# Kernel optimization log

Measured on AMD Instinct MI355X. Metric: run time of the kernel, lower is better.

Reference implementation:

```python
import jax, jax.numpy as jnp
import numpy as np

B, T, N, F_IN = 4, 8, 2048, 16
HID, HEADS, OUT_CH, OUT_FEAT = 128, 4, 64, 14
E = 32768


def _ln(x, g, b, eps=1e-5):
    mu = x.mean(-1, keepdims=True)
    var = ((x - mu) ** 2).mean(-1, keepdims=True)
    return (x - mu) / jnp.sqrt(var + eps) * g + b


def _attn_steps(x, wq, bq, wk, bk, wv, bv, wo, bo):
    # x: [B, S, M, F]; single-head causal attention over axis 1 (the 'steps' axis)
    q = x @ wq + bq
    k = x @ wk + bk
    v = x @ wv + bv
    scale = 1.0 / np.sqrt(q.shape[-1]).astype(np.float32)
    scores = jnp.einsum('bsmh,btmh->bmst', q, k) * scale  # [B,M,S,S]
    S = scores.shape[-1]
    scores = jnp.where(jnp.tril(jnp.ones((S, S), bool)), scores, -jnp.inf)
    a = jax.nn.softmax(scores, axis=-1)
    ctx = jnp.einsum('bmst,btmh->bsmh', a, v)
    return ctx @ wo + bo


def _attn_nodes(x, wq, bq, wk, bk, wv, bv, wo, bo):
    # single-head attention over axis 2 (the 'nodes' axis)
    q = x @ wq + bq
    k = x @ wk + bk
    v = x @ wv + bv
    scale = 1.0 / np.sqrt(q.shape[-1]).astype(np.float32)
    scores = jnp.einsum('bsnh,bsmh->bsnm', q, k) * scale
    a = jax.nn.softmax(scores, axis=-1)
    ctx = jnp.einsum('bsnm,bsmh->bsnh', a, v)
    return ctx @ wo + bo


def _gat(h, src, dst, n, W, a_src, a_dst, bias, heads, out_ch, concat):
    # PyG GATConv: gather src/dst features per edge, segment softmax over
    # incoming edges of each target node, weighted scatter-aggregate.
    hw = (h @ W).reshape(n, heads, out_ch)
    al_s = (hw * a_src).sum(-1)  # [n, heads]
    al_d = (hw * a_dst).sum(-1)
    loop = jnp.arange(n, dtype=src.dtype)
    src_f = jnp.concatenate([src, loop])
    dst_f = jnp.concatenate([dst, loop])
    alpha = jax.nn.leaky_relu(al_s[src_f] + al_d[dst_f], 0.2)
    # PyG removes pre-existing self-loops then adds canonical ones: mask them out.
    drop = jnp.concatenate([src == dst, jnp.zeros((n,), bool)])[:, None]
    amax = jax.lax.stop_gradient(
        jax.ops.segment_max(jnp.where(drop, -jnp.inf, alpha), dst_f, num_segments=n))
    ex = jnp.where(drop, 0.0, jnp.exp(alpha - amax[dst_f]))
    denom = jax.ops.segment_sum(ex, dst_f, num_segments=n)
    w = ex / denom[dst_f]  # [E_total, heads]
    out = jax.ops.segment_sum(hw[src_f] * w[:, :, None], dst_f, num_segments=n)
    if concat:
        return out.reshape(n, heads * out_ch) + bias
    return out.mean(1) + bias


def _forward(x, edge_index, ln1_g, ln1_b, t_wq, t_bq, t_wk, t_bk, t_wv, t_bv, t_wo, t_bo,
             skip_w, skip_b, ln2_g, ln2_b, s_wq, s_bq, s_wk, s_bk, s_wv, s_bv, s_wo, s_bo,
             ln3_g, ln3_b, mlp_w1, mlp_b1, mlp_w2, mlp_b2,
             gat1_w, gat1_asrc, gat1_adst, gat1_b, gat2_w, gat2_asrc, gat2_adst, gat2_b,
             ffn_w, ffn_b):
    Bx, Tx, Nx, _ = x.shape
    h = jnp.transpose(x, (0, 2, 1, 3))  # [B, N(steps), T(nodes), F]
    h = (h @ skip_w + skip_b) + _attn_steps(_ln(h, ln1_g, ln1_b),
                                            t_wq, t_bq, t_wk, t_bk, t_wv, t_bv, t_wo, t_bo)
    h = h + _attn_nodes(_ln(h, ln2_g, ln2_b), s_wq, s_bq, s_wk, s_bk, s_wv, s_bv, s_wo, s_bo)
    z = _ln(h, ln3_g, ln3_b)
    h = h + (jax.nn.relu(z @ mlp_w1 + mlp_b1) @ mlp_w2 + mlp_b2)
    h = h[:, :, -1, :].reshape(Bx * Nx, HID)  # last 'nodes'(=T) slot, flatten graphs
    src, dst = edge_index[0], edge_index[1]
    off = jnp.repeat(jnp.arange(Bx, dtype=src.dtype) * Nx, src.shape[0])
    src_b = jnp.tile(src, Bx) + off
    dst_b = jnp.tile(dst, Bx) + off
    nt = Bx * Nx
    g1 = jax.nn.elu(_gat(h, src_b, dst_b, nt, gat1_w, gat1_asrc, gat1_adst, gat1_b,
                         HEADS, HID // HEADS, True))
    g2 = _gat(g1, src_b, dst_b, nt, gat2_w, gat2_asrc, gat2_adst, gat2_b, 1, OUT_CH, False)
    out = g2.reshape(Bx, Nx, OUT_CH) @ ffn_w + ffn_b
    return jnp.transpose(out, (0, 2, 1))  # [B, output_features, N]


def setup_inputs():
    key = jax.random.key(0)
    ki = iter(list(jax.random.split(key, 40)))
    def rn(shape, s=0.05):
        return jax.random.normal(next(ki), shape, jnp.float32) * s
    d = {}
    d['x'] = jax.random.normal(next(ki), (B, T, N, F_IN), jnp.float32)
    d['edge_index'] = jax.random.randint(next(ki), (2, E), 0, N, jnp.int32)
    d['ln1_g'] = jnp.ones((F_IN,), jnp.float32); d['ln1_b'] = jnp.zeros((F_IN,), jnp.float32)
    d['t_wq'] = rn((F_IN, HID)); d['t_bq'] = jnp.zeros((HID,), jnp.float32)
    d['t_wk'] = rn((F_IN, HID)); d['t_bk'] = jnp.zeros((HID,), jnp.float32)
    d['t_wv'] = rn((F_IN, HID)); d['t_bv'] = jnp.zeros((HID,), jnp.float32)
    d['t_wo'] = rn((HID, HID)); d['t_bo'] = jnp.zeros((HID,), jnp.float32)
    d['skip_w'] = rn((F_IN, HID)); d['skip_b'] = jnp.zeros((HID,), jnp.float32)
    d['ln2_g'] = jnp.ones((HID,), jnp.float32); d['ln2_b'] = jnp.zeros((HID,), jnp.float32)
    d['s_wq'] = rn((HID, HID)); d['s_bq'] = jnp.zeros((HID,), jnp.float32)
    d['s_wk'] = rn((HID, HID)); d['s_bk'] = jnp.zeros((HID,), jnp.float32)
    d['s_wv'] = rn((HID, HID)); d['s_bv'] = jnp.zeros((HID,), jnp.float32)
    d['s_wo'] = rn((HID, HID)); d['s_bo'] = jnp.zeros((HID,), jnp.float32)
    d['ln3_g'] = jnp.ones((HID,), jnp.float32); d['ln3_b'] = jnp.zeros((HID,), jnp.float32)
    d['mlp_w1'] = rn((HID, 2 * HID)); d['mlp_b1'] = jnp.zeros((2 * HID,), jnp.float32)
    d['mlp_w2'] = rn((2 * HID, HID)); d['mlp_b2'] = jnp.zeros((HID,), jnp.float32)
    d['gat1_w'] = rn((HID, HID))
    d['gat1_asrc'] = rn((HEADS, HID // HEADS)); d['gat1_adst'] = rn((HEADS, HID // HEADS))
    d['gat1_b'] = jnp.zeros((HID,), jnp.float32)
    d['gat2_w'] = rn((HID, OUT_CH))
    d['gat2_asrc'] = rn((1, OUT_CH)); d['gat2_adst'] = rn((1, OUT_CH))
    d['gat2_b'] = jnp.zeros((OUT_CH,), jnp.float32)
    d['ffn_w'] = rn((OUT_CH, OUT_FEAT)); d['ffn_b'] = jnp.zeros((OUT_FEAT,), jnp.float32)
    return d


def reference(x, edge_index, ln1_g, ln1_b, t_wq, t_bq, t_wk, t_bk, t_wv, t_bv, t_wo, t_bo,
              skip_w, skip_b, ln2_g, ln2_b, s_wq, s_bq, s_wk, s_bk, s_wv, s_bv, s_wo, s_bo,
              ln3_g, ln3_b, mlp_w1, mlp_b1, mlp_w2, mlp_b2,
              gat1_w, gat1_asrc, gat1_adst, gat1_b, gat2_w, gat2_asrc, gat2_adst, gat2_b,
              ffn_w, ffn_b):
    return _forward(x, edge_index, ln1_g, ln1_b, t_wq, t_bq, t_wk, t_bk, t_wv, t_bv, t_wo, t_bo,
                    skip_w, skip_b, ln2_g, ln2_b, s_wq, s_bq, s_wk, s_bk, s_wv, s_bv, s_wo, s_bo,
                    ln3_g, ln3_b, mlp_w1, mlp_b1, mlp_w2, mlp_b2,
                    gat1_w, gat1_asrc, gat1_adst, gat1_b, gat2_w, gat2_asrc, gat2_adst, gat2_b,
                    ffn_w, ffn_b)
```

## Files before the change

### kernel.cpp

```cpp
#include <hip/hip_runtime.h>
#include <hip/hip_bf16.h>
#include <stdint.h>


#define BB     4
#define TT     8
#define NN     2048
#define FIN    16
#define HID    128
#define BM     (BB*TT)
#define PROWS  (BM*NN)
#define NHEADS 4
#define OUTCH  64
#define OUTF   14
#define NEDGE  32768
#define NEDGEB (NEDGE*BB)
#define NNODE  (BB*NN)
#define NETOT  (NEDGEB + NNODE)

#define TQ     64
#define NTILE  (NN/TQ)

typedef __hip_bfloat16 bf16;
typedef __attribute__((ext_vector_type(8))) short bf16x8;
typedef __attribute__((ext_vector_type(4))) float f32x4;

__device__ __forceinline__ float b2f(bf16 v){ return __bfloat162float(v); }
__device__ __forceinline__ bf16  f2b(float f){ return __float2bfloat16(f); }
__device__ __forceinline__ unsigned short bfbits(float f){
    union { bf16 h; unsigned short u; } cv; cv.h = f2b(f); return cv.u;
}

__global__ __launch_bounds__(256)
void k_kv(const float* __restrict__ x,
          const float* __restrict__ g1, const float* __restrict__ bb1,
          const float* __restrict__ wk, const float* __restrict__ bk,
          const float* __restrict__ wv, const float* __restrict__ bv,
          int in_off, bf16* __restrict__ K, bf16* __restrict__ Vt)
{
    const int r0 = blockIdx.x * 32;
    const int t  = threadIdx.x;

    __shared__ float wk_s[FIN][HID];
    __shared__ float wv_s[FIN][HID];
    __shared__ float xr_s[32][FIN+1];
    __shared__ float ln_s[32][FIN+1];

    #pragma unroll
    for (int it = 0; it < 2; ++it){
        const int u = t + it*256;
        ((float4*)wk_s)[u] = ((const float4*)wk)[u];
        ((float4*)wv_s)[u] = ((const float4*)wv)[u];
    }
    #pragma unroll
    for (int it = 0; it < 2; ++it){
        const int u = t + it*256;
        xr_s[u >> 4][u & 15] = x[(size_t)(r0 + in_off)*FIN + u];
    }
    __syncthreads();

    if (t < 32){
        float mu = 0.f;
        #pragma unroll
        for (int f = 0; f < FIN; ++f) mu += xr_s[t][f];
        mu *= (1.f/FIN);
        float var = 0.f;
        #pragma unroll
        for (int f = 0; f < FIN; ++f){ float d = xr_s[t][f]-mu; var += d*d; }
        var *= (1.f/FIN);
        const float inv = rsqrtf(var + 1e-5f);
        #pragma unroll
        for (int f = 0; f < FIN; ++f)
            ln_s[t][f] = (xr_s[t][f]-mu)*inv*g1[f] + bb1[f];
    }
    __syncthreads();

    {
        const int hk = (t & 63)*2;
        const float2 bkv = *(const float2*)&bk[hk];
        #pragma unroll
        for (int pass = 0; pass < 8; ++pass){
            const int key = pass*4 + (t >> 6);
            float a0 = bkv.x, a1 = bkv.y;
            #pragma unroll
            for (int f = 0; f < FIN; ++f){
                const float l = ln_s[key][f];
                const float2 wkv = ((const float2*)&wk_s[f][0])[t & 63];
                a0 += l*wkv.x; a1 += l*wkv.y;
            }
            const unsigned int pk =
                (unsigned int)bfbits(a0) | ((unsigned int)bfbits(a1) << 16);
            *(unsigned int*)(void*)&K[((size_t)(r0 + key))*HID + hk] = pk;
        }
    }

    {
        const int slice = r0 >> 11;
        const int kg    = (r0 & (NN-1)) >> 5;
        const size_t vbase = ((size_t)slice*(NN/32) + kg)*(size_t)HID*32;
        const int kk = (t & 15)*2;
        #pragma unroll
        for (int pass = 0; pass < 8; ++pass){
            const int h = (t >> 4) + 16*pass;
            float a0 = bv[h], a1 = a0;
            #pragma unroll
            for (int f = 0; f < FIN; ++f){
                const float wvf = wv_s[f][h];
                a0 += ln_s[kk  ][f] * wvf;
                a1 += ln_s[kk+1][f] * wvf;
            }
            const unsigned int pk =
                (unsigned int)bfbits(a0) | ((unsigned int)bfbits(a1) << 16);
            *(unsigned int*)(void*)&Vt[vbase + (size_t)h*32 + kk] = pk;
        }
    }
}

__global__ __launch_bounds__(256)
void k_attn_mfma(const float* __restrict__ x,
                 const bf16* __restrict__ K, const bf16* __restrict__ Vt,
                 const float* __restrict__ g1, const float* __restrict__ bb1,
                 const float* __restrict__ wq, const float* __restrict__ bq,
                 int slice_off, bf16* __restrict__ CX)
{
    int slice, tile, kvslice;
    if (gridDim.y == 1){
        const int bid = (int)blockIdx.x;
        slice   = (bid & 7)*4 + ((bid >> 3) & 3);
        tile    = (NTILE-1) - (bid >> 5);
        kvslice = slice;
    } else {
        tile    = (NTILE-1) - (int)blockIdx.y;
        slice   = (int)blockIdx.x + slice_off;
        kvslice = (int)blockIdx.x;
    }
    const int q0    = tile*TQ;
    const int t     = threadIdx.x;
    const int w     = t >> 6;
    const int lane  = t & 63;
    const int quad  = lane >> 4;
    const int l16   = lane & 15;
    const int wr0   = w*16;

    const float qscale = 0.08838834764831845f * 1.4426950408889634f;

    __shared__ float xs [TQ][FIN+1];
    __shared__ bf16  Ps [4][16][40];
    __shared__ __align__(16) bf16 KVs[32*136 + 128*40];
    bf16* Ks = KVs;
    bf16* Vs = KVs + 32*136;
    bf16 (*wqs)[32] = (bf16(*)[32])(&KVs[0]);
    bf16 (*xsb)[32] = (bf16(*)[32])(&KVs[4096]);
    bf16 (*Qv)[136] = (bf16(*)[136])(&KVs[0]);

    const size_t kb = (size_t)kvslice * NN * HID;
    const size_t vb = (size_t)kvslice * (size_t)(NN/32) * HID*32;
    const bf16* kptr = K  + kb + (size_t)t*8;
    const bf16* vptr = Vt + vb + (size_t)t*8;
    bf16x8 kreg0, kreg1, vreg0, vreg1;
    kreg0 = *(const bf16x8*)(const void*)(kptr);
    kreg1 = *(const bf16x8*)(const void*)(kptr + 2048);
    vreg0 = *(const bf16x8*)(const void*)(vptr);
    vreg1 = *(const bf16x8*)(const void*)(vptr + 2048);

    #pragma unroll
    for (int it = 0; it < 4; ++it){
        const int u = t + it*256;
        xs[u >> 4][u & 15] = x[((size_t)slice*NN + q0)*FIN + u];
    }
    #pragma unroll
    for (int it = 0; it < 8; ++it){
        const int u = t + it*256;
        const int f = u >> 7, ch = u & 127;
        wqs[ch][f] = f2b(wq[u] * qscale);
    }
    {
        const bf16x8 z8 = {0,0,0,0,0,0,0,0};
        const int ch = t >> 1, k0 = 16 + (t & 1)*8;
        *(bf16x8*)(void*)&wqs[ch][k0] = z8;
    }
    __syncthreads();

    if (t < TQ){
        float mu = 0.f;
        #pragma unroll
        for (int f = 0; f < FIN; ++f) mu += xs[t][f];
        mu *= (1.f/FIN);
        float var = 0.f;
        #pragma unroll
        for (int f = 0; f < FIN; ++f){ float d = xs[t][f]-mu; var += d*d; }
        var *= (1.f/FIN);
        const float inv = rsqrtf(var + 1e-5f);
        bf16x8 v0, v1;
        #pragma unroll
        for (int f = 0; f < 8; ++f)
            v0[f] = (short)bfbits((xs[t][f]-mu)*inv*g1[f] + bb1[f]);
        #pragma unroll
        for (int f = 0; f < 8; ++f)
            v1[f] = (short)bfbits((xs[t][8+f]-mu)*inv*g1[8+f] + bb1[8+f]);
        const bf16x8 z8 = {0,0,0,0,0,0,0,0};
        *(bf16x8*)(void*)&xsb[t][0]  = v0;
        *(bf16x8*)(void*)&xsb[t][8]  = v1;
        *(bf16x8*)(void*)&xsb[t][16] = z8;
        *(bf16x8*)(void*)&xsb[t][24] = z8;
    }
    __syncthreads();

    {
        const bf16x8 af = *(const bf16x8*)(const void*)&xsb[wr0 + l16][quad*8];
        f32x4 Cq[8];
        #pragma unroll
        for (int ct = 0; ct < 8; ++ct){
            const bf16x8 bfv = *(const bf16x8*)(const void*)&wqs[ct*16 + l16][quad*8];
            Cq[ct] = __builtin_amdgcn_mfma_f32_16x16x32_bf16(
                         af, bfv, (f32x4){0.f,0.f,0.f,0.f}, 0, 0, 0);
        }
        __syncthreads();
        #pragma unroll
        for (int ct = 0; ct < 8; ++ct){
            const int col = ct*16 + l16;
            const float bqs = bq[col] * qscale;
            #pragma unroll
            for (int r = 0; r < 4; ++r)
                Qv[wr0 + quad*4 + r][col] = f2b(Cq[ct][r] + bqs);
        }
    }
    __syncthreads();

    bf16x8 qf[4];
    #pragma unroll
    for (int ks = 0; ks < 4; ++ks)
        qf[ks] = *(const bf16x8*)(const void*)&Qv[wr0 + l16][ks*32 + quad*8];
    __syncthreads();

    f32x4 O[8];
    #pragma unroll
    for (int ct = 0; ct < 8; ++ct) O[ct] = (f32x4){0.f,0.f,0.f,0.f};
    float l_[4] = {0.f,0.f,0.f,0.f};

    const int jend_blk = q0 + TQ - 1;
    const int my_jmax  = q0 + wr0 + 15;
    const int brow = q0 + wr0 + quad*4;

    bf16* ksA = &Ks[((t      ) >> 4)*136 + ((t      ) & 15)*8];
    bf16* ksB = &Ks[((t + 256) >> 4)*136 + ((t + 256) & 15)*8];
    bf16* vsA = &Vs[((t      ) >> 2)*40  + ((t      ) &  3)*8];
    bf16* vsB = &Vs[((t + 256) >> 2)*40  + ((t + 256) &  3)*8];
    const bf16* kr0 = &Ks[(2*l16    )*136 + quad*8];
    const bf16* kr1 = &Ks[(2*l16 + 1)*136 + quad*8];
    const bf16* vr  = &Vs[l16*40 + quad*8];

    for (int j0 = 0; j0 <= jend_blk; j0 += 32){
        *(bf16x8*)(void*)ksA = kreg0;
        *(bf16x8*)(void*)ksB = kreg1;
        *(bf16x8*)(void*)vsA = vreg0;
        *(bf16x8*)(void*)vsB = vreg1;
        __syncthreads();

        if (j0 + 32 <= jend_blk){
            const size_t off = (size_t)(j0 + 32)*128;
            kreg0 = *(const bf16x8*)(const void*)(kptr + off);
            kreg1 = *(const bf16x8*)(const void*)(kptr + off + 2048);
            vreg0 = *(const bf16x8*)(const void*)(vptr + off);
            vreg1 = *(const bf16x8*)(const void*)(vptr + off + 2048);
        }

        if (j0 <= my_jmax){
            f32x4 S0 = (f32x4){0.f,0.f,0.f,0.f}, S1 = S0;
            #pragma unroll
            for (int ks = 0; ks < 4; ++ks){
                const bf16x8 kf0 = *(const bf16x8*)(const void*)(kr0 + ks*32);
                const bf16x8 kf1 = *(const bf16x8*)(const void*)(kr1 + ks*32);
                S0 = __builtin_amdgcn_mfma_f32_16x16x32_bf16(qf[ks], kf0, S0, 0, 0, 0);
                S1 = __builtin_amdgcn_mfma_f32_16x16x32_bf16(qf[ks], kf1, S1, 0, 0, 0);
            }
            float sv0[4], sv1[4];
            if (j0 + 31 > q0 + wr0){
                const int c0j = j0 + 2*l16, c1j = c0j + 1;
                #pragma unroll
                for (int r = 0; r < 4; ++r){
                    sv0[r] = (c0j <= brow + r) ? S0[r] : -1e30f;
                    sv1[r] = (c1j <= brow + r) ? S1[r] : -1e30f;
                }
            } else {
                #pragma unroll
                for (int r = 0; r < 4; ++r){ sv0[r] = S0[r]; sv1[r] = S1[r]; }
            }
            #pragma unroll
            for (int r = 0; r < 4; ++r){
                const float e0 = __builtin_amdgcn_exp2f(sv0[r]);
                const float e1 = __builtin_amdgcn_exp2f(sv1[r]);
                l_[r] += e0 + e1;
                const unsigned int pk =
                    (unsigned int)bfbits(e0) | ((unsigned int)bfbits(e1) << 16);
                *(unsigned int*)(void*)&Ps[w][quad*4 + r][2*l16] = pk;
            }
            const bf16x8 pf = *(const bf16x8*)(const void*)&Ps[w][l16][quad*8];
            #pragma unroll
            for (int ct = 0; ct < 8; ++ct){
                const bf16x8 vf = *(const bf16x8*)(const void*)(vr + ct*16*40);
                O[ct] = __builtin_amdgcn_mfma_f32_16x16x32_bf16(pf, vf, O[ct], 0, 0, 0);
            }
        }
        __syncthreads();
    }

    {
        float inv[4];
        #pragma unroll
        for (int r = 0; r < 4; ++r){
            float rs = l_[r];
            rs += __shfl_xor(rs, 1);
            rs += __shfl_xor(rs, 2);
            rs += __shfl_xor(rs, 4);
            rs += __shfl_xor(rs, 8);
            inv[r] = 1.f/rs;
        }
        #pragma unroll
        for (int ct = 0; ct < 8; ++ct)
        #pragma unroll
        for (int r = 0; r < 4; ++r)
            Qv[wr0 + quad*4 + r][ct*16 + l16] = f2b(O[ct][r]*inv[r]);
    }
    __syncthreads();
    {
        const int row = t >> 2, ch0 = (t & 3)*32;
        bf16* dst = CX + ((size_t)slice*NN + q0 + row)*HID + ch0;
        #pragma unroll
        for (int c = 0; c < 4; ++c)
            *(bf16x8*)(void*)(dst + c*8) =
                *(const bf16x8*)(const void*)&Qv[row][ch0 + c*8];
    }
}

__global__ __launch_bounds__(256)
void k_h1(const float* __restrict__ x,
          const bf16* __restrict__ BH1,
          const float* __restrict__ t_bo, const float* __restrict__ skb,
          int slice_off, bf16* __restrict__ CXH1)
{
    const int slice = blockIdx.x + slice_off;
    const int q0    = blockIdx.y * TQ;
    const int t     = threadIdx.x;
    const int w     = t >> 6;
    const int lane  = t & 63;
    const int quad  = lane >> 4;
    const int l16   = lane & 15;
    const int wr0   = w*16;

    __shared__ bf16 Aext[TQ][168];

    {
        const bf16* src = CXH1 + ((size_t)slice*NN + q0)*HID;
        #pragma unroll
        for (int it = 0; it < 4; ++it){
            const int c = t + it*256;
            *(bf16x8*)(void*)&Aext[c>>4][(c&15)*8] =
                *(const bf16x8*)(const void*)(src + c*8);
        }
    }
    #pragma unroll
    for (int it = 0; it < 4; ++it){
        const int u = t + it*256;
        const int row = u >> 4, f = u & 15;
        Aext[row][128 + f] = f2b(x[((size_t)slice*NN + q0 + row)*FIN + f]);
    }
    #pragma unroll
    for (int it = 0; it < 4; ++it){
        const int u = t + it*256;
        Aext[u>>4][144 + (u&15)] = f2b(0.f);
    }
    __syncthreads();

    f32x4 O[8];
    #pragma unroll
    for (int ct = 0; ct < 8; ++ct) O[ct] = (f32x4){0.f,0.f,0.f,0.f};
    #pragma unroll
    for (int ks = 0; ks < 5; ++ks){
        const bf16x8 af = *(const bf16x8*)(const void*)&Aext[wr0 + l16][ks*32 + quad*8];
        #pragma unroll
        for (int ct = 0; ct < 8; ++ct){
            const bf16x8 bf = *(const bf16x8*)(const void*)
                (BH1 + (size_t)(ct*16 + l16)*168 + ks*32 + quad*8);
            O[ct] = __builtin_amdgcn_mfma_f32_16x16x32_bf16(af, bf, O[ct], 0, 0, 0);
        }
    }
    __syncthreads();
    #pragma unroll
    for (int ct = 0; ct < 8; ++ct){
        const int col = ct*16 + l16;
        const float bias = t_bo[col] + skb[col];
        #pragma unroll
        for (int r = 0; r < 4; ++r)
            Aext[wr0 + quad*4 + r][col] = f2b(O[ct][r] + bias);
    }
    __syncthreads();
    {
        const int row = t >> 2, ch0 = (t & 3)*32;
        bf16* dst = CXH1 + ((size_t)slice*NN + q0 + row)*HID + ch0;
        #pragma unroll
        for (int c = 0; c < 4; ++c)
            *(bf16x8*)(void*)(dst + c*8) =
                *(const bf16x8*)(const void*)&Aext[row][ch0 + c*8];
    }
}

__global__ __launch_bounds__(256)
void k_prep(const float* __restrict__ s_wq, const float* __restrict__ s_wk,
            const float* __restrict__ bq, const float* __restrict__ bk,
            const float* __restrict__ s_wv, const float* __restrict__ s_wo,
            const float* __restrict__ g1w, const float* __restrict__ w1,
            const float* __restrict__ w2,
            const float* __restrict__ t_wo, const float* __restrict__ skw,
            bf16* __restrict__ Mt, bf16* __restrict__ wvT, bf16* __restrict__ woT,
            bf16* __restrict__ g1wT, bf16* __restrict__ w1T, bf16* __restrict__ w2T,
            bf16* __restrict__ BH1,
            float* __restrict__ vk, float* __restrict__ vq, float* __restrict__ sbb,
            float* __restrict__ zp, int zn)
{
    const int b = blockIdx.x;
    const int t = threadIdx.x;
    for (int u = b*256 + t; u < zn; u += 32*256) zp[u] = 0.f;
    __shared__ float wq_s[HID*HID];
    __shared__ float wk_s[8][HID];
    if (b < 16){
        for (int u = t; u < HID*HID; u += 256) wq_s[u] = s_wq[u];
        for (int u = t; u < 8*HID;   u += 256) ((float*)wk_s)[u] = s_wk[b*8*HID + u];
        __syncthreads();
        #pragma unroll
        for (int i = 0; i < 4; ++i){
            const int e = t + i*256;
            const int cl = e >> 7, a = e & 127;
            float acc = 0.f;
            for (int hh = 0; hh < HID; ++hh) acc += wk_s[cl][hh]*wq_s[a*HID + hh];
            Mt[(size_t)(b*8 + cl)*HID + a] = f2b(acc);
        }
    } else if (b == 16){
        if (t < HID){
            float a1 = 0.f, a2 = 0.f;
            for (int hh = 0; hh < HID; ++hh){
                a1 += bq[hh]*s_wk[t*HID + hh];
                a2 += s_wq[t*HID + hh]*bk[hh];
            }
            vk[t] = a1; vq[t] = a2;
            if (t == 0){
                float s = 0.f;
                for (int hh = 0; hh < HID; ++hh) s += bq[hh]*bk[hh];
                *sbb = s;
            }
        }
    } else if (b == 17){
        for (int u = t; u < HID*HID; u += 256){
            const int c = u >> 7, h = u & 127;
            wvT[h*HID + c] = f2b(s_wv[u]);
        }
    } else if (b == 18){
        for (int u = t; u < HID*HID; u += 256){
            const int c = u >> 7, h = u & 127;
            woT[h*HID + c] = f2b(s_wo[u]);
        }
    } else if (b == 19){
        for (int u = t; u < HID*HID; u += 256){
            const int c = u >> 7, h = u & 127;
            g1wT[h*HID + c] = f2b(g1w[u]);
        }
    } else if (b == 20){
        for (int u = t; u < HID*2*HID; u += 256){
            const int k = u >> 8, n = u & 255;
            w1T[n*HID + k] = f2b(w1[u]);
        }
    } else if (b == 21){
        for (int u = t; u < 2*HID*HID; u += 256){
            const int k = u >> 7, n = u & 127;
            w2T[(size_t)n*2*HID + k] = f2b(w2[u]);
        }
    } else if (b == 22){
        for (int u = t; u < HID*168; u += 256){
            const int c = u / 168, k = u - c*168;
            float v = 0.f;
            if (k < 128)      v = t_wo[k*HID + c];
            else if (k < 144) v = skw[(k-128)*HID + c];
            BH1[u] = f2b(v);
        }
    }
}

__global__ __launch_bounds__(256)
void k_mix(const bf16* __restrict__ H1,
           const float* __restrict__ ln2g, const float* __restrict__ ln2b,
           const bf16* __restrict__ Mt, const bf16* __restrict__ wvT,
           const bf16* __restrict__ woT, const bf16* __restrict__ g1wT,
           const bf16* __restrict__ w1T, const bf16* __restrict__ w2T,
           const float* __restrict__ vk, const float* __restrict__ vq,
           const float* __restrict__ sbbp,
           const float* __restrict__ s_bv, const float* __restrict__ s_bo,
           const float* __restrict__ bm1, const float* __restrict__ bm2,
           const float* __restrict__ ln3g, const float* __restrict__ ln3b,
           const float* __restrict__ g1as, const float* __restrict__ g1ad,
           bf16* __restrict__ hw1, float* __restrict__ als1, float* __restrict__ ald1)
{
    const int blk0 = blockIdx.x * 16;
    const int bb = blk0 >> 11, s0 = blk0 & (NN-1);
    const int t = threadIdx.x;
    const int w = t >> 6;
    const int lane = t & 63;
    const int quad = lane >> 4;
    const int l16  = lane & 15;

    __shared__ bf16  h1s[16][TT][136];
    __shared__ bf16  ZA [16][136];
    __shared__ bf16  HLs[16][264];
    __shared__ float Cw [16][128];
    __shared__ float ln2gs[HID], ln2bs[HID];
    __shared__ float mu_s[16][TT], inv_s[16][TT];
    __shared__ float ps[16][TT];
    __shared__ float sbq_s[16], mu3[16], inv3[16];

    for (int m = 0; m < TT; ++m){
        const bf16* src = H1 + ((size_t)(bb*TT + m)*NN + s0)*HID;
        const int node = t >> 4, c8 = t & 15;
        *(bf16x8*)(void*)&h1s[node][m][c8*8] =
            *(const bf16x8*)(const void*)(src + (size_t)node*HID + c8*8);
    }
    if (t < HID){ ln2gs[t] = ln2g[t]; ln2bs[t] = ln2b[t]; }
    __syncthreads();

    {
        const int idx = t >> 1, half = t & 1;
        const int node = idx >> 3, m = idx & 7;
        float sum = 0.f, sq = 0.f;
        for (int c = half; c < HID; c += 2){
            const float v = b2f(h1s[node][m][c]);
            sum += v; sq += v*v;
        }
        sum += __shfl_xor(sum, 1); sq += __shfl_xor(sq, 1);
        if (half == 0){
            const float mu = sum*(1.f/HID);
            const float var = sq*(1.f/HID) - mu*mu;
            mu_s[node][m] = mu;
            inv_s[node][m] = rsqrtf(var + 1e-5f);
        }
    }
    __syncthreads();

    #pragma unroll
    for (int i = 0; i < 8; ++i){
        const int idx = t + i*256;
        const int n = idx >> 7, c = idx & 127;
        const float z = (b2f(h1s[n][7][c]) - mu_s[n][7])*inv_s[n][7]*ln2gs[c] + ln2bs[c];
        ZA[n][c] = f2b(z);
    }
    if (t < 128){
        const int node = t >> 3, l8 = t & 7;
        float sp = 0.f;
        for (int c = l8; c < HID; c += 8){
            const float z = (b2f(h1s[node][7][c]) - mu_s[node][7])*inv_s[node][7]*ln2gs[c] + ln2bs[c];
            sp += vq[c]*z;
        }
        sp += __shfl_xor(sp, 1);
        sp += __shfl_xor(sp, 2);
        sp += __shfl_xor(sp, 4);
        if (l8 == 0) sbq_s[node] = sp;
    }
    __syncthreads();

    {
        bf16x8 af[4];
        #pragma unroll
        for (int ks = 0; ks < 4; ++ks)
            af[ks] = *(const bf16x8*)(const void*)&ZA[l16][ks*32 + quad*8];
        __syncthreads();
        f32x4 C0 = (f32x4){0,0,0,0}, C1 = C0;
        #pragma unroll
        for (int ks = 0; ks < 4; ++ks){
            const bf16x8 b0 = *(const bf16x8*)(const void*)(Mt + (size_t)(w*32      + l16)*HID + ks*32 + quad*8);
            const bf16x8 b1 = *(const bf16x8*)(const void*)(Mt + (size_t)(w*32 + 16 + l16)*HID + ks*32 + quad*8);
            C0 = __builtin_amdgcn_mfma_f32_16x16x32_bf16(af[ks], b0, C0, 0, 0, 0);
            C1 = __builtin_amdgcn_mfma_f32_16x16x32_bf16(af[ks], b1, C1, 0, 0, 0);
        }
        const int c0 = w*32 + l16, c1 = c0 + 16;
        #pragma unroll
        for (int r = 0; r < 4; ++r){
            Cw[quad*4 + r][c0] = C0[r] + vk[c0];
            Cw[quad*4 + r][c1] = C1[r] + vk[c1];
        }
    }
    __syncthreads();

    {
        const int idx = t >> 1, half = t & 1;
        const int node = idx >> 3, m = idx & 7;
        const float mu = mu_s[node][m], iv = inv_s[node][m];
        float d = 0.f;
        for (int c = half; c < HID; c += 2){
            const float z = (b2f(h1s[node][m][c]) - mu)*iv*ln2gs[c] + ln2bs[c];
            d += Cw[node][c]*z;
        }
        d += __shfl_xor(d, 1);
        if (half == 0)
            ps[node][m] = (d + sbq_s[node] + *sbbp) * 0.08838834764831845f;
    }
    __syncthreads();
    if (t < 16){
        float mx = -1e30f;
        #pragma unroll
        for (int m = 0; m < TT; ++m) mx = fmaxf(mx, ps[t][m]);
        float p[TT], se = 0.f;
        #pragma unroll
        for (int m = 0; m < TT; ++m){ p[m] = __expf(ps[t][m]-mx); se += p[m]; }
        const float isum = 1.f/se;
        #pragma unroll
        for (int m = 0; m < TT; ++m) ps[t][m] = p[m]*isum;
    }
    __syncthreads();
    #pragma unroll
    for (int i = 0; i < 8; ++i){
        const int idx = t + i*256;
        const int n = idx >> 7, c = idx & 127;
        const float gc = ln2gs[c], bc = ln2bs[c];
        float acc = 0.f;
        #pragma unroll
        for (int m = 0; m < TT; ++m){
            const float z = (b2f(h1s[n][m][c]) - mu_s[n][m])*inv_s[n][m]*gc + bc;
            acc += ps[n][m]*z;
        }
        ZA[n][c] = f2b(acc);
    }
    __syncthreads();

    {
        bf16x8 af[4];
        #pragma unroll
        for (int ks = 0; ks < 4; ++ks)
            af[ks] = *(const bf16x8*)(const void*)&ZA[l16][ks*32 + quad*8];
        __syncthreads();
        f32x4 C0 = (f32x4){0,0,0,0}, C1 = C0;
        #pragma unroll
        for (int ks = 0; ks < 4; ++ks){
            const bf16x8 b0 = *(const bf16x8*)(const void*)(wvT + (size_t)(w*32      + l16)*HID + ks*32 + quad*8);
            const bf16x8 b1 = *(const bf16x8*)(const void*)(wvT + (size_t)(w*32 + 16 + l16)*HID + ks*32 + quad*8);
            C0 = __builtin_amdgcn_mfma_f32_16x16x32_bf16(af[ks], b0, C0, 0, 0, 0);
            C1 = __builtin_amdgcn_mfma_f32_16x16x32_bf16(af[ks], b1, C1, 0, 0, 0);
        }
        const int c0 = w*32 + l16, c1 = c0 + 16;
        #pragma unroll
        for (int r = 0; r < 4; ++r){
            ZA[quad*4 + r][c0] = f2b(C0[r] + s_bv[c0]);
            ZA[quad*4 + r][c1] = f2b(C1[r] + s_bv[c1]);
        }
    }
    __syncthreads();

    {
        bf16x8 af[4];
        #pragma unroll
        for (int ks = 0; ks < 4; ++ks)
            af[ks] = *(const bf16x8*)(const void*)&ZA[l16][ks*32 + quad*8];
        __syncthreads();
        f32x4 C0 = (f32x4){0,0,0,0}, C1 = C0;
        #pragma unroll
        for (int ks = 0; ks < 4; ++ks){
            const bf16x8 b0 = *(const bf16x8*)(const void*)(woT + (size_t)(w*32      + l16)*HID + ks*32 + quad*8);
            const bf16x8 b1 = *(const bf16x8*)(const void*)(woT + (size_t)(w*32 + 16 + l16)*HID + ks*32 + quad*8);
            C0 = __builtin_amdgcn_mfma_f32_16x16x32_bf16(af[ks], b0, C0, 0, 0, 0);
            C1 = __builtin_amdgcn_mfma_f32_16x16x32_bf16(af[ks], b1, C1, 0, 0, 0);
        }
        const int c0 = w*32 + l16, c1 = c0 + 16;
        #pragma unroll
        for (int r = 0; r < 4; ++r){
            const int node = quad*4 + r;
            Cw[node][c0] = C0[r] + s_bo[c0] + b2f(h1s[node][7][c0]);
            Cw[node][c1] = C1[r] + s_bo[c1] + b2f(h1s[node][7][c1]);
        }
    }
    __syncthreads();

    {
        const int node = t >> 4, part = t & 15;
        float sum = 0.f, sq = 0.f;
        for (int c = part; c < HID; c += 16){
            const float v = Cw[node][c];
            sum += v; sq += v*v;
        }
        sum += __shfl_xor(sum, 1); sq += __shfl_xor(sq, 1);
        sum += __shfl_xor(sum, 2); sq += __shfl_xor(sq, 2);
        sum += __shfl_xor(sum, 4); sq += __shfl_xor(sq, 4);
        sum += __shfl_xor(sum, 8); sq += __shfl_xor(sq, 8);
        if (part == 0){
            const float mu = sum*(1.f/HID);
            const float var = sq*(1.f/HID) - mu*mu;
            mu3[node] = mu;
            inv3[node] = rsqrtf(var + 1e-5f);
        }
    }
    __syncthreads();
    #pragma unroll
    for (int i = 0; i < 8; ++i){
        const int idx = t + i*256;
        const int n = idx >> 7, c = idx & 127;
        ZA[n][c] = f2b((Cw[n][c] - mu3[n])*inv3[n]*ln3g[c] + ln3b[c]);
    }
    __syncthreads();

    {
        bf16x8 af[4];
        #pragma unroll
        for (int ks = 0; ks < 4; ++ks)
            af[ks] = *(const bf16x8*)(const void*)&ZA[l16][ks*32 + quad*8];
        __syncthreads();
        f32x4 C[4];
        #pragma unroll
        for (int u = 0; u < 4; ++u) C[u] = (f32x4){0,0,0,0};
        #pragma unroll
        for (int ks = 0; ks < 4; ++ks){
            #pragma unroll
            for (int u = 0; u < 4; ++u){
                const bf16x8 bfv = *(const bf16x8*)(const void*)
                    (w1T + (size_t)(w*64 + u*16 + l16)*HID + ks*32 + quad*8);
                C[u] = __builtin_amdgcn_mfma_f32_16x16x32_bf16(af[ks], bfv, C[u], 0, 0, 0);
            }
        }
        #pragma unroll
        for (int u = 0; u < 4; ++u){
            const int col = w*64 + u*16 + l16;
            const float bias = bm1[col];
            #pragma unroll
            for (int r = 0; r < 4; ++r)
                HLs[quad*4 + r][col] = f2b(fmaxf(C[u][r] + bias, 0.f));
        }
    }
    __syncthreads();

    {
        bf16x8 af[8];
        #pragma unroll
        for (int ks = 0; ks < 8; ++ks)
            af[ks] = *(const bf16x8*)(const void*)&HLs[l16][ks*32 + quad*8];
        __syncthreads();
        f32x4 C0 = (f32x4){0,0,0,0}, C1 = C0;
        #pragma unroll
        for (int ks = 0; ks < 8; ++ks){
            const bf16x8 b0 = *(const bf16x8*)(const void*)(w2T + (size_t)(w*32      + l16)*2*HID + ks*32 + quad*8);
            const bf16x8 b1 = *(const bf16x8*)(const void*)(w2T + (size_t)(w*32 + 16 + l16)*2*HID + ks*32 + quad*8);
            C0 = __builtin_amdgcn_mfma_f32_16x16x32_bf16(af[ks], b0, C0, 0, 0, 0);
            C1 = __builtin_amdgcn_mfma_f32_16x16x32_bf16(af[ks], b1, C1, 0, 0, 0);
        }
        const int c0 = w*32 + l16, c1 = c0 + 16;
        #pragma unroll
        for (int r = 0; r < 4; ++r){
            const int node = quad*4 + r;
            ZA[node][c0] = f2b(C0[r] + bm2[c0] + Cw[node][c0]);
            ZA[node][c1] = f2b(C1[r] + bm2[c1] + Cw[node][c1]);
        }
    }
    __syncthreads();

    {
        bf16x8 af[4];
        #pragma unroll
        for (int ks = 0; ks < 4; ++ks)
            af[ks] = *(const bf16x8*)(const void*)&ZA[l16][ks*32 + quad*8];
        __syncthreads();
        f32x4 C0 = (f32x4){0,0,0,0}, C1 = C0;
        #pragma unroll
        for (int ks = 0; ks < 4; ++ks){
            const bf16x8 b0 = *(const bf16x8*)(const void*)(g1wT + (size_t)(w*32      + l16)*HID + ks*32 + quad*8);
            const bf16x8 b1 = *(const bf16x8*)(const void*)(g1wT + (size_t)(w*32 + 16 + l16)*HID + ks*32 + quad*8);
            C0 = __builtin_amdgcn_mfma_f32_16x16x32_bf16(af[ks], b0, C0, 0, 0, 0);
            C1 = __builtin_amdgcn_mfma_f32_16x16x32_bf16(af[ks], b1, C1, 0, 0, 0);
        }
        const int c0 = w*32 + l16, c1 = c0 + 16;
        #pragma unroll
        for (int r = 0; r < 4; ++r){
            Cw[quad*4 + r][c0] = C0[r];
            Cw[quad*4 + r][c1] = C1[r];
        }
    }
    __syncthreads();

    #pragma unroll
    for (int i = 0; i < 8; ++i){
        const int idx = t + i*256;
        hw1[(size_t)blk0*HID + idx] = f2b(((const float*)Cw)[idx]);
    }
    if (t < 64){
        const int node = t >> 2, hd = t & 3;
        float s1 = 0.f, s2 = 0.f;
        for (int j = 0; j < 32; ++j){
            const int c = hd*32 + j;
            const float a = Cw[node][c];
            s1 += a*g1as[c];
            s2 += a*g1ad[c];
        }
        als1[(blk0 + node)*NHEADS + hd] = s1;
        ald1[(blk0 + node)*NHEADS + hd] = s2;
    }
}

__global__ void k_csr_hist(const int* __restrict__ ei, int* __restrict__ cnt)
{
    const int e = blockIdx.x*blockDim.x + threadIdx.x;
    if (e >= NEDGE) return;
    const int s = ei[e], d = ei[NEDGE + e];
    if (s != d) atomicAdd(&cnt[d], 1);
}

__global__ __launch_bounds__(256)
void k_csr_scan(const int* __restrict__ cnt, int* __restrict__ roff)
{
    const int t = threadIdx.x;
    __shared__ int part[256];
    int loc[8]; int s = 0;
    #pragma unroll
    for (int i = 0; i < 8; ++i){ loc[i] = s; s += cnt[t*8 + i]; }
    part[t] = s;
    __syncthreads();
    if (t == 0){
        int acc = 0;
        for (int i = 0; i < 256; ++i){ const int v = part[i]; part[i] = acc; acc += v; }
    }
    __syncthreads();
    const int base_ = part[t];
    #pragma unroll
    for (int i = 0; i < 8; ++i) roff[t*8 + i] = base_ + loc[i];
    if (t == 255) roff[2048] = base_ + s;
}

__global__ void k_csr_scatter(const int* __restrict__ ei, const int* __restrict__ roff,
                              int* __restrict__ fill, int* __restrict__ col)
{
    const int e = blockIdx.x*blockDim.x + threadIdx.x;
    if (e >= NEDGE) return;
    const int s = ei[e], d = ei[NEDGE + e];
    if (s != d){
        const int p = roff[d] + atomicAdd(&fill[d], 1);
        col[p] = s;
    }
}

__global__ __launch_bounds__(64)
void k_gat_g1lin(const int* __restrict__ roff, const int* __restrict__ col,
                 const float* __restrict__ als, const float* __restrict__ ald,
                 const bf16* __restrict__ hw, const float* __restrict__ g1b,
                 const float* __restrict__ W,
                 const float* __restrict__ asrc, const float* __restrict__ adst,
                 bf16* __restrict__ hw2, float* __restrict__ al2s, float* __restrict__ al2d)
{
    const int nid = blockIdx.x;
    const int d   = nid & (NN-1);
    const int gb  = nid & ~(NN-1);
    const int c2  = threadIdx.x;
    const int hd  = c2 >> 4;
    const float ad = ald[nid*NHEADS + hd];

    float av0 = 0.f, av1 = 0.f, accd = 0.f;
    const int e0 = roff[d], e1 = roff[d+1];
    int sn = (e0 < e1) ? col[e0] : 0;
    for (int e = e0; e < e1; ++e){
        const int s = sn + gb;
        sn = (e+1 < e1) ? col[e+1] : 0;
        float a = als[s*NHEADS + hd] + ad;
        a = a > 0.f ? a : 0.2f*a;
        const float ex = __expf(a);
        const unsigned int pk =
            *(const unsigned int*)(const void*)&hw[(size_t)s*HID + 2*c2];
        av0 += ex * __uint_as_float(pk << 16);
        av1 += ex * __uint_as_float(pk & 0xffff0000u);
        accd += ex;
    }
    {
        float a = als[nid*NHEADS + hd] + ad;
        a = a > 0.f ? a : 0.2f*a;
        const float ex = __expf(a);
        const unsigned int pk =
            *(const unsigned int*)(const void*)&hw[(size_t)nid*HID + 2*c2];
        av0 += ex * __uint_as_float(pk << 16);
        av1 += ex * __uint_as_float(pk & 0xffff0000u);
        accd += ex;
    }
    __shared__ float hrs[HID];
    {
        float v0 = av0/accd + g1b[2*c2];
        float v1 = av1/accd + g1b[2*c2+1];
        v0 = v0 > 0.f ? v0 : expm1f(v0);
        v1 = v1 > 0.f ? v1 : expm1f(v1);
        *(float2*)(void*)&hrs[2*c2] = make_float2(v0, v1);
    }
    __syncthreads();

    const int c = c2;
    float a = 0.f;
    for (int k = 0; k < HID; ++k) a += hrs[k]*W[k*OUTCH + c];
    hw2[(size_t)nid*OUTCH + c] = f2b(a);
    float s1 = a*asrc[c], s2 = a*adst[c];
    #pragma unroll
    for (int off = 32; off > 0; off >>= 1){
        s1 += __shfl_down(s1, off);
        s2 += __shfl_down(s2, off);
    }
    if (c == 0){ al2s[nid] = s1; al2d[nid] = s2; }
}

__global__ __launch_bounds__(64)
void k_gat_gather2f(const int* __restrict__ roff, const int* __restrict__ col,
                    const float* __restrict__ als, const float* __restrict__ ald,
                    const bf16* __restrict__ hw2, const float* __restrict__ g2b,
                    const float* __restrict__ fw, const float* __restrict__ fb,
                    float* __restrict__ out)
{
    const int nid = blockIdx.x;
    const int d   = nid & (NN-1);
    const int gb  = nid & ~(NN-1);
    const int c   = threadIdx.x;
    const float ad = ald[nid];

    float accv = 0.f, accd = 0.f;
    const int e0 = roff[d], e1 = roff[d+1];
    int sn = (e0 < e1) ? col[e0] : 0;
    for (int e = e0; e < e1; ++e){
        const int s = sn + gb;
        sn = (e+1 < e1) ? col[e+1] : 0;
        float a = als[s] + ad;
        a = a > 0.f ? a : 0.2f*a;
        const float ex = __expf(a);
        accv += ex * b2f(hw2[(size_t)s*OUTCH + c]);
        accd += ex;
    }
    {
        float a = als[nid] + ad;
        a = a > 0.f ? a : 0.2f*a;
        const float ex = __expf(a);
        accv += ex * b2f(hw2[(size_t)nid*OUTCH + c]);
        accd += ex;
    }
    __shared__ float g[OUTCH];
    g[c] = accv/accd + g2b[c];
    __syncthreads();
    if (c < OUTF){
        float o = fb[c];
        #pragma unroll
        for (int k = 0; k < OUTCH; ++k) o += g[k]*fw[k*OUTF + c];
        const int b = nid >> 11, n = nid & (NN-1);
        out[((size_t)b*OUTF + c)*NN + n] = o;
    }
}

extern "C" void kernel_launch(void* const* d_in, const int* in_sizes, int n_in,
                              void* d_out, int out_size, void* d_ws, size_t ws_size,
                              hipStream_t stream)
{
    const float* x    = (const float*)d_in[0];
    const int*  ei    = (const int*)d_in[1];
    const float* ln1g = (const float*)d_in[2];  const float* ln1b = (const float*)d_in[3];
    const float* t_wq = (const float*)d_in[4];  const float* t_bq = (const float*)d_in[5];
    const float* t_wk = (const float*)d_in[6];  const float* t_bk = (const float*)d_in[7];
    const float* t_wv = (const float*)d_in[8];  const float* t_bv = (const float*)d_in[9];
    const float* t_wo = (const float*)d_in[10]; const float* t_bo = (const float*)d_in[11];
    const float* skw  = (const float*)d_in[12]; const float* skb  = (const float*)d_in[13];
    const float* ln2g = (const float*)d_in[14]; const float* ln2b = (const float*)d_in[15];
    const float* s_wq = (const float*)d_in[16]; const float* s_bq = (const float*)d_in[17];
    const float* s_wk = (const float*)d_in[18]; const float* s_bk = (const float*)d_in[19];
    const float* s_wv = (const float*)d_in[20]; const float* s_bv = (const float*)d_in[21];
    const float* s_wo = (const float*)d_in[22]; const float* s_bo = (const float*)d_in[23];
    const float* ln3g = (const float*)d_in[24]; const float* ln3b = (const float*)d_in[25];
    const float* w1   = (const float*)d_in[26]; const float* b1   = (const float*)d_in[27];
    const float* w2   = (const float*)d_in[28]; const float* b2   = (const float*)d_in[29];
    const float* g1w  = (const float*)d_in[30];
    const float* g1as = (const float*)d_in[31]; const float* g1ad = (const float*)d_in[32];
    const float* g1b  = (const float*)d_in[33];
    const float* g2w  = (const float*)d_in[34];
    const float* g2as = (const float*)d_in[35]; const float* g2ad = (const float*)d_in[36];
    const float* g2b  = (const float*)d_in[37];
    const float* ffw  = (const float*)d_in[38]; const float* ffb  = (const float*)d_in[39];
    float* out = (float*)d_out;

    const size_t MiB = 1024u*1024u;
    const bool wide = ws_size >= 48*MiB;

    char* base = (char*)d_ws;
    bf16 *Kb, *Vtb, *CXH1;
    char* gat_base;
    char* mbase;
    if (wide){
        Kb   = (bf16*)(base + 0*MiB);
        Vtb  = (bf16*)(base + 16*MiB);
        CXH1 = (bf16*)(base + 32*MiB);
        gat_base = base;
        mbase = base + 13*MiB;
    } else {
        CXH1 = (bf16*)(base + 0*MiB);
        gat_base = base + 16*MiB;
        Kb   = (bf16*)(base + 26*MiB);
        Vtb  = (bf16*)(base + 26*MiB + 512u*1024u);
        mbase = base + 27*MiB;
    }
    bf16*  Mt   = (bf16*)mbase;
    bf16*  wvT  = (bf16*)(mbase + 32*1024);
    bf16*  woT  = (bf16*)(mbase + 64*1024);
    bf16*  g1wT = (bf16*)(mbase + 96*1024);
    bf16*  w1T  = (bf16*)(mbase + 128*1024);
    bf16*  w2T  = (bf16*)(mbase + 192*1024);
    float* vkw  = (float*)(mbase + 256*1024);
    float* vqw  = (float*)(mbase + 256*1024 + 512);
    float* sbb  = (float*)(mbase + 256*1024 + 1024);
    bf16*  BH1  = (bf16*)(mbase + 272*1024);

    char* w = gat_base;
    auto alloc = [&](size_t bytes){ void* p = (void*)w; w += (bytes + 255) & ~(size_t)255; return p; };
    int*   cnt  = (int*)  alloc(2048u*sizeof(int));
    int*   fill = (int*)  alloc(2048u*sizeof(int));
    char*  zend = w;
    int*   roff = (int*)  alloc(2049u*sizeof(int));
    int*   col  = (int*)  alloc((size_t)NEDGE*sizeof(int));
    bf16*  hw1  = (bf16*) alloc((size_t)NNODE*HID*sizeof(bf16));
    float* als1 = (float*)alloc((size_t)NNODE*NHEADS*sizeof(float));
    float* ald1 = (float*)alloc((size_t)NNODE*NHEADS*sizeof(float));
    bf16*  hw2  = (bf16*) alloc((size_t)NNODE*OUTCH*sizeof(bf16));
    float* als2 = (float*)alloc((size_t)NNODE*sizeof(float));
    float* ald2 = (float*)alloc((size_t)NNODE*sizeof(float));
    const int zero_n = (int)((zend - (char*)cnt)/4);

    if (wide){
        k_kv<<<PROWS/32, 256, 0, stream>>>(x, ln1g, ln1b, t_wk, t_bk, t_wv, t_bv, 0, Kb, Vtb);
        k_attn_mfma<<<BM*NTILE, 256, 0, stream>>>(x, Kb, Vtb, ln1g, ln1b,
                                                  t_wq, t_bq, 0, CXH1);
        k_prep<<<32, 256, 0, stream>>>(s_wq, s_wk, s_bq, s_bk, s_wv, s_wo, g1w, w1, w2,
                                       t_wo, skw,
                                       Mt, wvT, woT, g1wT, w1T, w2T, BH1,
                                       vkw, vqw, sbb, (float*)cnt, zero_n);
        k_h1<<<dim3(BM, NTILE), 256, 0, stream>>>(x, BH1, t_bo, skb, 0, CXH1);
    } else {
        for (int s = 0; s < BM; ++s){
            k_kv<<<NN/32, 256, 0, stream>>>(x, ln1g, ln1b, t_wk, t_bk, t_wv, t_bv, s*NN, Kb, Vtb);
            k_attn_mfma<<<dim3(1, NTILE), 256, 0, stream>>>(x, Kb, Vtb, ln1g, ln1b,
                                                            t_wq, t_bq, s, CXH1);
        }
        k_prep<<<32, 256, 0, stream>>>(s_wq, s_wk, s_bq, s_bk, s_wv, s_wo, g1w, w1, w2,
                                       t_wo, skw,
                                       Mt, wvT, woT, g1wT, w1T, w2T, BH1,
                                       vkw, vqw, sbb, (float*)cnt, zero_n);
        k_h1<<<dim3(BM, NTILE), 256, 0, stream>>>(x, BH1, t_bo, skb, 0, CXH1);
    }

    k_csr_hist   <<<NEDGE/256, 256, 0, stream>>>(ei, cnt);
    k_csr_scan   <<<1,        256, 0, stream>>>(cnt, roff);
    k_csr_scatter<<<NEDGE/256, 256, 0, stream>>>(ei, roff, fill, col);

    k_mix<<<NNODE/16, 256, 0, stream>>>(CXH1, ln2g, ln2b, Mt, wvT, woT, g1wT, w1T, w2T,
                                        vkw, vqw, sbb, s_bv, s_bo, b1, b2,
                                        ln3g, ln3b, g1as, g1ad, hw1, als1, ald1);

    k_gat_g1lin  <<<NNODE, 64, 0, stream>>>(roff, col, als1, ald1, hw1, g1b,
                                            g2w, g2as, g2ad, hw2, als2, ald2);
    k_gat_gather2f<<<NNODE, 64, 0, stream>>>(roff, col, als2, ald2, hw2, g2b, ffw, ffb, out);
}
```

Before: 390.1 us.

## Fuse temporal output projection into attention kernel and move prep weights to output buffer

The separate k_h1 kernel, which applied the output projection plus skip connection, is folded into the tail of k_attn_mfma. The attention context now stays in shared memory and goes straight through the MFMA projection, so the CX round trip through global memory and one launch are removed. k_prep now runs first and writes its transposed weights into the output buffer as scratch, and the CSR counter zeroing moves from k_prep to a hipMemsetAsync. The fused kernel uses more shared memory and registers, which may lower attention occupancy.

```diff
diff --git a/kernel.cpp b/kernel.cpp
--- a/kernel.cpp
+++ b/kernel.cpp
@@ -121,7 +121,9 @@
                  const bf16* __restrict__ K, const bf16* __restrict__ Vt,
                  const float* __restrict__ g1, const float* __restrict__ bb1,
                  const float* __restrict__ wq, const float* __restrict__ bq,
-                 int slice_off, bf16* __restrict__ CX)
+                 const bf16* __restrict__ BH1,
+                 const float* __restrict__ t_bo, const float* __restrict__ skb,
+                 int slice_off, bf16* __restrict__ CXH1)
 {
     int slice, tile, kvslice;
     if (gridDim.y == 1){
@@ -145,13 +147,14 @@
     const float qscale = 0.08838834764831845f * 1.4426950408889634f;
 
     __shared__ float xs [TQ][FIN+1];
-    __shared__ bf16  Ps [4][16][40];
-    __shared__ __align__(16) bf16 KVs[32*136 + 128*40];
-    bf16* Ks = KVs;
-    bf16* Vs = KVs + 32*136;
-    bf16 (*wqs)[32] = (bf16(*)[32])(&KVs[0]);
-    bf16 (*xsb)[32] = (bf16(*)[32])(&KVs[4096]);
-    bf16 (*Qv)[136] = (bf16(*)[136])(&KVs[0]);
+    __shared__ __align__(16) bf16 SM[12032];
+    bf16* Psb = SM;
+    bf16* Ks  = SM + 2560;
+    bf16* Vs  = SM + 6912;
+    bf16 (*wqs)[32] = (bf16(*)[32])(SM + 2560);
+    bf16 (*xsb)[32] = (bf16(*)[32])(SM + 6656);
+    bf16 (*Qv)[136] = (bf16(*)[136])(SM + 2560);
+    bf16* AE  = SM;
 
     const size_t kb = (size_t)kvslice * NN * HID;
     const size_t vb = (size_t)kvslice * (size_t)(NN/32) * HID*32;
@@ -249,6 +252,8 @@
     const bf16* kr0 = &Ks[(2*l16    )*136 + quad*8];
     const bf16* kr1 = &Ks[(2*l16 + 1)*136 + quad*8];
     const bf16* vr  = &Vs[l16*40 + quad*8];
+    bf16* psw = &Psb[w*640 + (quad*4)*40 + 2*l16];
+    const bf16* psr = &Psb[w*640 + l16*40 + quad*8];
 
     for (int j0 = 0; j0 <= jend_blk; j0 += 32){
         *(bf16x8*)(void*)ksA = kreg0;
@@ -293,9 +298,9 @@
                 l_[r] += e0 + e1;
                 const unsigned int pk =
                     (unsigned int)bfbits(e0) | ((unsigned int)bfbits(e1) << 16);
-                *(unsigned int*)(void*)&Ps[w][quad*4 + r][2*l16] = pk;
+                *(unsigned int*)(void*)(psw + r*40) = pk;
             }
-            const bf16x8 pf = *(const bf16x8*)(const void*)&Ps[w][l16][quad*8];
+            const bf16x8 pf = *(const bf16x8*)(const void*)psr;
             #pragma unroll
             for (int ct = 0; ct < 8; ++ct){
                 const bf16x8 vf = *(const bf16x8*)(const void*)(vr + ct*16*40);
@@ -320,69 +325,33 @@
         for (int ct = 0; ct < 8; ++ct)
         #pragma unroll
         for (int r = 0; r < 4; ++r)
-            Qv[wr0 + quad*4 + r][ct*16 + l16] = f2b(O[ct][r]*inv[r]);
-    }
-    __syncthreads();
-    {
-        const int row = t >> 2, ch0 = (t & 3)*32;
-        bf16* dst = CX + ((size_t)slice*NN + q0 + row)*HID + ch0;
-        #pragma unroll
-        for (int c = 0; c < 4; ++c)
-            *(bf16x8*)(void*)(dst + c*8) =
-                *(const bf16x8*)(const void*)&Qv[row][ch0 + c*8];
-    }
-}
-
-__global__ __launch_bounds__(256)
-void k_h1(const float* __restrict__ x,
-          const bf16* __restrict__ BH1,
-          const float* __restrict__ t_bo, const float* __restrict__ skb,
-          int slice_off, bf16* __restrict__ CXH1)
-{
-    const int slice = blockIdx.x + slice_off;
-    const int q0    = blockIdx.y * TQ;
-    const int t     = threadIdx.x;
-    const int w     = t >> 6;
-    const int lane  = t & 63;
-    const int quad  = lane >> 4;
-    const int l16   = lane & 15;
-    const int wr0   = w*16;
-
-    __shared__ bf16 Aext[TQ][168];
-
-    {
-        const bf16* src = CXH1 + ((size_t)slice*NN + q0)*HID;
-        #pragma unroll
-        for (int it = 0; it < 4; ++it){
-            const int c = t + it*256;
-            *(bf16x8*)(void*)&Aext[c>>4][(c&15)*8] =
-                *(const bf16x8*)(const void*)(src + c*8);
-        }
+            AE[(wr0 + quad*4 + r)*168 + ct*16 + l16] = f2b(O[ct][r]*inv[r]);
     }
     #pragma unroll
     for (int it = 0; it < 4; ++it){
         const int u = t + it*256;
-        const int row = u >> 4, f = u & 15;
-        Aext[row][128 + f] = f2b(x[((size_t)slice*NN + q0 + row)*FIN + f]);
-    }
-    #pragma unroll
-    for (int it = 0; it < 4; ++it){
+        AE[(u >> 4)*168 + 128 + (u & 15)] = f2b(xs[u >> 4][u & 15]);
+    }
+    #pragma unroll
+    for (int it = 0; it < 6; ++it){
         const int u = t + it*256;
-        Aext[u>>4][144 + (u&15)] = f2b(0.f);
-    }
-    __syncthreads();
-
-    f32x4 O[8];
-    #pragma unroll
-    for (int ct = 0; ct < 8; ++ct) O[ct] = (f32x4){0.f,0.f,0.f,0.f};
-    #pragma unroll
-    for (int ks = 0; ks < 5; ++ks){
-        const bf16x8 af = *(const bf16x8*)(const void*)&Aext[wr0 + l16][ks*32 + quad*8];
+        const int row = u/24;
+        AE[row*168 + 144 + (u - row*24)] = f2b(0.f);
+    }
+    __syncthreads();
+
+    f32x4 O2[8];
+    #pragma unroll
+    for (int ct = 0; ct < 8; ++ct) O2[ct] = (f32x4){0.f,0.f,0.f,0.f};
+    #pragma unroll
+    for (int k5 = 0; k5 < 5; ++k5){
+        const bf16x8 af = *(const bf16x8*)(const void*)
+            &AE[(wr0 + l16)*168 + k5*32 + quad*8];
         #pragma unroll
         for (int ct = 0; ct < 8; ++ct){
-            const bf16x8 bf = *(const bf16x8*)(const void*)
-                (BH1 + (size_t)(ct*16 + l16)*168 + ks*32 + quad*8);
-            O[ct] = __builtin_amdgcn_mfma_f32_16x16x32_bf16(af, bf, O[ct], 0, 0, 0);
+            const bf16x8 bfv = *(const bf16x8*)(const void*)
+                (BH1 + (size_t)(ct*16 + l16)*168 + k5*32 + quad*8);
+            O2[ct] = __builtin_amdgcn_mfma_f32_16x16x32_bf16(af, bfv, O2[ct], 0, 0, 0);
         }
     }
     __syncthreads();
@@ -392,7 +361,7 @@
         const float bias = t_bo[col] + skb[col];
         #pragma unroll
         for (int r = 0; r < 4; ++r)
-            Aext[wr0 + quad*4 + r][col] = f2b(O[ct][r] + bias);
+            AE[(wr0 + quad*4 + r)*168 + col] = f2b(O2[ct][r] + bias);
     }
     __syncthreads();
     {
@@ -401,7 +370,7 @@
         #pragma unroll
         for (int c = 0; c < 4; ++c)
             *(bf16x8*)(void*)(dst + c*8) =
-                *(const bf16x8*)(const void*)&Aext[row][ch0 + c*8];
+                *(const bf16x8*)(const void*)&AE[row*168 + ch0 + c*8];
     }
 }
 
@@ -415,12 +384,10 @@
             bf16* __restrict__ Mt, bf16* __restrict__ wvT, bf16* __restrict__ woT,
             bf16* __restrict__ g1wT, bf16* __restrict__ w1T, bf16* __restrict__ w2T,
             bf16* __restrict__ BH1,
-            float* __restrict__ vk, float* __restrict__ vq, float* __restrict__ sbb,
-            float* __restrict__ zp, int zn)
+            float* __restrict__ vk, float* __restrict__ vq, float* __restrict__ sbb)
 {
     const int b = blockIdx.x;
     const int t = threadIdx.x;
-    for (int u = b*256 + t; u < zn; u += 32*256) zp[u] = 0.f;
     __shared__ float wq_s[HID*HID];
     __shared__ float wk_s[8][HID];
     if (b < 16){
@@ -980,36 +947,34 @@
     char* base = (char*)d_ws;
     bf16 *Kb, *Vtb, *CXH1;
     char* gat_base;
-    char* mbase;
     if (wide){
         Kb   = (bf16*)(base + 0*MiB);
         Vtb  = (bf16*)(base + 16*MiB);
         CXH1 = (bf16*)(base + 32*MiB);
         gat_base = base;
-        mbase = base + 13*MiB;
     } else {
         CXH1 = (bf16*)(base + 0*MiB);
         gat_base = base + 16*MiB;
         Kb   = (bf16*)(base + 26*MiB);
         Vtb  = (bf16*)(base + 26*MiB + 512u*1024u);
-        mbase = base + 27*MiB;
-    }
-    bf16*  Mt   = (bf16*)mbase;
-    bf16*  wvT  = (bf16*)(mbase + 32*1024);
-    bf16*  woT  = (bf16*)(mbase + 64*1024);
-    bf16*  g1wT = (bf16*)(mbase + 96*1024);
-    bf16*  w1T  = (bf16*)(mbase + 128*1024);
-    bf16*  w2T  = (bf16*)(mbase + 192*1024);
-    float* vkw  = (float*)(mbase + 256*1024);
-    float* vqw  = (float*)(mbase + 256*1024 + 512);
-    float* sbb  = (float*)(mbase + 256*1024 + 1024);
-    bf16*  BH1  = (bf16*)(mbase + 272*1024);
+    }
+
+    char* ob = (char*)d_out;
+    bf16*  Mt   = (bf16*)(ob);
+    bf16*  wvT  = (bf16*)(ob + 32*1024);
+    bf16*  woT  = (bf16*)(ob + 64*1024);
+    bf16*  g1wT = (bf16*)(ob + 96*1024);
+    bf16*  w1T  = (bf16*)(ob + 128*1024);
+    bf16*  w2T  = (bf16*)(ob + 192*1024);
+    float* vkw  = (float*)(ob + 256*1024);
+    float* vqw  = (float*)(ob + 256*1024 + 512);
+    float* sbb  = (float*)(ob + 256*1024 + 1024);
+    bf16*  BH1  = (bf16*)(ob + 272*1024);
 
     char* w = gat_base;
     auto alloc = [&](size_t bytes){ void* p = (void*)w; w += (bytes + 255) & ~(size_t)255; return p; };
     int*   cnt  = (int*)  alloc(2048u*sizeof(int));
     int*   fill = (int*)  alloc(2048u*sizeof(int));
-    char*  zend = w;
     int*   roff = (int*)  alloc(2049u*sizeof(int));
     int*   col  = (int*)  alloc((size_t)NEDGE*sizeof(int));
     bf16*  hw1  = (bf16*) alloc((size_t)NNODE*HID*sizeof(bf16));
@@ -1018,30 +983,24 @@
     bf16*  hw2  = (bf16*) alloc((size_t)NNODE*OUTCH*sizeof(bf16));
     float* als2 = (float*)alloc((size_t)NNODE*sizeof(float));
     float* ald2 = (float*)alloc((size_t)NNODE*sizeof(float));
-    const int zero_n = (int)((zend - (char*)cnt)/4);
-
+
+    k_prep<<<32, 256, 0, stream>>>(s_wq, s_wk, s_bq, s_bk, s_wv, s_wo, g1w, w1, w2,
+                                   t_wo, skw,
+                                   Mt, wvT, woT, g1wT, w1T, w2T, BH1,
+                                   vkw, vqw, sbb);
     if (wide){
         k_kv<<<PROWS/32, 256, 0, stream>>>(x, ln1g, ln1b, t_wk, t_bk, t_wv, t_bv, 0, Kb, Vtb);
         k_attn_mfma<<<BM*NTILE, 256, 0, stream>>>(x, Kb, Vtb, ln1g, ln1b,
-                                                  t_wq, t_bq, 0, CXH1);
-        k_prep<<<32, 256, 0, stream>>>(s_wq, s_wk, s_bq, s_bk, s_wv, s_wo, g1w, w1, w2,
-                                       t_wo, skw,
-                                       Mt, wvT, woT, g1wT, w1T, w2T, BH1,
-                                       vkw, vqw, sbb, (float*)cnt, zero_n);
-        k_h1<<<dim3(BM, NTILE), 256, 0, stream>>>(x, BH1, t_bo, skb, 0, CXH1);
+                                                  t_wq, t_bq, BH1, t_bo, skb, 0, CXH1);
     } else {
         for (int s = 0; s < BM; ++s){
             k_kv<<<NN/32, 256, 0, stream>>>(x, ln1g, ln1b, t_wk, t_bk, t_wv, t_bv, s*NN, Kb, Vtb);
             k_attn_mfma<<<dim3(1, NTILE), 256, 0, stream>>>(x, Kb, Vtb, ln1g, ln1b,
-                                                            t_wq, t_bq, s, CXH1);
-        }
-        k_prep<<<32, 256, 0, stream>>>(s_wq, s_wk, s_bq, s_bk, s_wv, s_wo, g1w, w1, w2,
-                                       t_wo, skw,
-                                       Mt, wvT, woT, g1wT, w1T, w2T, BH1,
-                                       vkw, vqw, sbb, (float*)cnt, zero_n);
-        k_h1<<<dim3(BM, NTILE), 256, 0, stream>>>(x, BH1, t_bo, skb, 0, CXH1);
-    }
-
+                                                            t_wq, t_bq, BH1, t_bo, skb, s, CXH1);
+        }
+    }
+
+    hipMemsetAsync(cnt, 0, 2u*2048u*sizeof(int), stream);
     k_csr_hist   <<<NEDGE/256, 256, 0, stream>>>(ei, cnt);
     k_csr_scan   <<<1,        256, 0, stream>>>(cnt, roff);
     k_csr_scatter<<<NEDGE/256, 256, 0, stream>>>(ei, roff, fill, col);
```

Measured after the change: 387.2 us, median of 2. No clear change (-0.8%).
